# Kernel optimization log

Hardware: AMD Instinct MI355X
Metric: run time of the kernel (lower is better)

## Reference

```python
import jax, jax.numpy as jnp
import numpy as np

N_NODES = 100000
E = 1000000
IN_DIM = 64
HID = 64


def setup_inputs() -> dict:
    key = jax.random.key(0)
    ks = jax.random.split(key, 8)
    edge_emb = jax.random.normal(ks[0], (E, IN_DIM), dtype=jnp.float32)
    edge_indices = jax.random.randint(ks[1], (E, 2), 0, N_NODES, dtype=jnp.int64)
    s_in = 1.0 / np.sqrt(IN_DIM)
    s_h = 1.0 / np.sqrt(HID)
    Wf = jax.random.uniform(ks[2], (IN_DIM, HID), minval=-s_in, maxval=s_in, dtype=jnp.float32)
    bf = jax.random.uniform(ks[3], (HID,), minval=-s_in, maxval=s_in, dtype=jnp.float32)
    Wb = jax.random.uniform(ks[4], (IN_DIM, HID), minval=-s_in, maxval=s_in, dtype=jnp.float32)
    bb = jax.random.uniform(ks[5], (HID,), minval=-s_in, maxval=s_in, dtype=jnp.float32)
    Wg = jax.random.uniform(ks[6], (HID, 1), minval=-s_h, maxval=s_h, dtype=jnp.float32)
    bg = jax.random.uniform(ks[7], (1,), minval=-s_h, maxval=s_h, dtype=jnp.float32)
    return {"edge_emb": edge_emb, "Wf": Wf, "bf": bf, "Wb": Wb, "bb": bb,
            "Wg": Wg, "bg": bg, "edge_indices": edge_indices}


def reference(edge_emb, Wf, bf, Wb, bb, Wg, bg, edge_indices):
    u = edge_indices[:, 0]
    v = edge_indices[:, 1]
    # node_to_edges derived from incidence: sum of incident edge embeddings + degree
    node_sum = (jax.ops.segment_sum(edge_emb, u, num_segments=N_NODES)
                + jax.ops.segment_sum(edge_emb, v, num_segments=N_NODES))  # [N, d]
    ones = jnp.ones((edge_emb.shape[0],), edge_emb.dtype)
    deg = (jax.ops.segment_sum(ones, u, num_segments=N_NODES)
           + jax.ops.segment_sum(ones, v, num_segments=N_NODES))  # [N]

    def excl_mean(n):
        # mean over the node's incident edges excluding the current edge;
        # zeros when the current edge is the node's only incident edge.
        d = deg[n]                              # [E]
        s = node_sum[n] - edge_emb              # [E, d_in]
        denom = jnp.maximum(d - 1.0, 1.0)[:, None]
        return jnp.where((d > 1.0)[:, None], s / denom, jnp.zeros_like(s))

    agg_u = excl_mean(u)
    agg_v = excl_mean(v)
    agg_forward = agg_u @ Wf + bf               # [E, H]
    agg_backward = agg_v @ Wb + bb              # [E, H]
    gate = jax.nn.sigmoid((agg_forward + agg_backward) @ Wg + bg)  # [E, 1]
    return gate * agg_forward + (1.0 - gate) * agg_backward
```

## Files before the change

kernel.cpp:

```cpp
#include <hip/hip_runtime.h>
#include <hip/hip_bf16.h>
#include <math.h>

#define N_NODES 100000
#define DIM 64
#define BATCH 16
#define LDS_PITCH 72

typedef __attribute__((ext_vector_type(8))) short short8;
typedef __attribute__((ext_vector_type(4))) float floatx4;

__device__ __forceinline__ short f2bf(float x) {
    unsigned u = __float_as_uint(x);
    u += 0x7FFF + ((u >> 16) & 1);
    return (short)(u >> 16);
}
__device__ __forceinline__ float bf2f(unsigned short b) {
    return __uint_as_float(((unsigned)b) << 16);
}

__global__ __launch_bounds__(256) void scatter_kernel(
    const float* __restrict__ edge_emb, const int* __restrict__ idx,
    __hip_bfloat162* __restrict__ node_sum, float* __restrict__ deg, int n_edges)
{
    long long gid = (long long)blockIdx.x * blockDim.x + threadIdx.x;
    if (gid >= (long long)n_edges * 32) return;
    int e = (int)(gid >> 5);
    int p = (int)(gid & 31);
    float2 ev = ((const float2*)edge_emb)[gid];
    int2 uv = ((const int2*)idx)[e];
    union { unsigned u32; __hip_bfloat162 h; } cv;
    cv.u32 = (unsigned)(unsigned short)f2bf(ev.x)
           | ((unsigned)(unsigned short)f2bf(ev.y) << 16);
    unsafeAtomicAdd(&node_sum[(size_t)uv.x * 32 + p], cv.h);
    unsafeAtomicAdd(&node_sum[(size_t)uv.y * 32 + p], cv.h);
    if (p == 0) {
        unsafeAtomicAdd(&deg[uv.x], 1.f);
        unsafeAtomicAdd(&deg[uv.y], 1.f);
    }
}

__global__ __launch_bounds__(256) void fused_edge_kernel(
    const float* __restrict__ edge_emb,
    const int* __restrict__ idx,
    const unsigned short* __restrict__ node_sum,
    const float* __restrict__ deg,
    const float* __restrict__ Wf, const float* __restrict__ bf,
    const float* __restrict__ Wb, const float* __restrict__ bb,
    const float* __restrict__ Wg, const float* __restrict__ bg,
    float* __restrict__ out, int n_edges)
{
    __shared__ short lds[4][2][BATCH * LDS_PITCH];
    const int lane = threadIdx.x & 63;
    const int l15 = lane & 15;
    const int q = lane >> 4;
    const int wslot = threadIdx.x >> 6;
    const int wid = __builtin_amdgcn_readfirstlane(blockIdx.x * 4 + wslot);
    const int nwaves = gridDim.x * 4;

    short8 bWf[4][2], bWb[4][2];
#pragma unroll
    for (int nt = 0; nt < 4; ++nt)
#pragma unroll
        for (int kt = 0; kt < 2; ++kt) {
            short8 f, g;
#pragma unroll
            for (int j = 0; j < 8; ++j) {
                int k = kt * 32 + q * 8 + j;
                int n = nt * 16 + l15;
                f[j] = f2bf(Wf[k * 64 + n]);
                g[j] = f2bf(Wb[k * 64 + n]);
            }
            bWf[nt][kt] = f;
            bWb[nt][kt] = g;
        }
    float bfv[4], bbv[4], wgv[4];
#pragma unroll
    for (int nt = 0; nt < 4; ++nt) {
        bfv[nt] = bf[nt * 16 + l15];
        bbv[nt] = bb[nt * 16 + l15];
        wgv[nt] = Wg[nt * 16 + l15];
    }
    const float bgv = bg[0];

    short* ldsU = lds[wslot][0];
    short* ldsV = lds[wslot][1];

    const int nbatches = n_edges / BATCH;
    for (int b = wid; b < nbatches; b += nwaves) {
        const int e0 = b * BATCH;
#pragma unroll
        for (int i = 0; i < BATCH; ++i) {
            const int e = e0 + i;
            const int u = idx[2 * e];
            const int v = idx[2 * e + 1];
            const float du = deg[u];
            const float dv = deg[v];
            const float invu = (du > 1.f) ? 1.f / (du - 1.f) : 0.f;
            const float invv = (dv > 1.f) ? 1.f / (dv - 1.f) : 0.f;
            const float ev = edge_emb[(size_t)e * 64 + lane];
            const float nsu = bf2f(node_sum[(size_t)u * 64 + lane]);
            const float nsv = bf2f(node_sum[(size_t)v * 64 + lane]);
            ldsU[i * LDS_PITCH + lane] = f2bf((nsu - ev) * invu);
            ldsV[i * LDS_PITCH + lane] = f2bf((nsv - ev) * invv);
        }

        short8 aU[2], aV[2];
#pragma unroll
        for (int kt = 0; kt < 2; ++kt) {
            const int off = l15 * LDS_PITCH + kt * 32 + q * 8;
            aU[kt] = *(const short8*)&ldsU[off];
            aV[kt] = *(const short8*)&ldsV[off];
        }

        floatx4 cU[4], cV[4];
#pragma unroll
        for (int nt = 0; nt < 4; ++nt) {
            floatx4 z = {0.f, 0.f, 0.f, 0.f};
            z = __builtin_amdgcn_mfma_f32_16x16x32_bf16(aU[0], bWf[nt][0], z, 0, 0, 0);
            cU[nt] = __builtin_amdgcn_mfma_f32_16x16x32_bf16(aU[1], bWf[nt][1], z, 0, 0, 0);
            floatx4 z2 = {0.f, 0.f, 0.f, 0.f};
            z2 = __builtin_amdgcn_mfma_f32_16x16x32_bf16(aV[0], bWb[nt][0], z2, 0, 0, 0);
            cV[nt] = __builtin_amdgcn_mfma_f32_16x16x32_bf16(aV[1], bWb[nt][1], z2, 0, 0, 0);
        }

        float p[4] = {0.f, 0.f, 0.f, 0.f};
#pragma unroll
        for (int nt = 0; nt < 4; ++nt)
#pragma unroll
            for (int r = 0; r < 4; ++r) {
                float af = cU[nt][r] + bfv[nt];
                float ab = cV[nt][r] + bbv[nt];
                cU[nt][r] = af;
                cV[nt][r] = ab;
                p[r] = fmaf(af + ab, wgv[nt], p[r]);
            }
#pragma unroll
        for (int r = 0; r < 4; ++r) {
            float s = p[r];
            s += __shfl_xor(s, 1);
            s += __shfl_xor(s, 2);
            s += __shfl_xor(s, 4);
            s += __shfl_xor(s, 8);
            p[r] = 1.f / (1.f + __expf(-(s + bgv)));
        }
#pragma unroll
        for (int nt = 0; nt < 4; ++nt)
#pragma unroll
            for (int r = 0; r < 4; ++r) {
                const int e = e0 + q * 4 + r;
                out[(size_t)e * 64 + nt * 16 + l15] =
                    fmaf(p[r], cU[nt][r] - cV[nt][r], cV[nt][r]);
            }
    }
}

extern "C" void kernel_launch(void* const* d_in, const int* in_sizes, int n_in,
                              void* d_out, int out_size, void* d_ws, size_t ws_size,
                              hipStream_t stream) {
    const float* edge_emb = (const float*)d_in[0];
    const float* Wf = (const float*)d_in[1];
    const float* bf = (const float*)d_in[2];
    const float* Wb = (const float*)d_in[3];
    const float* bb = (const float*)d_in[4];
    const float* Wg = (const float*)d_in[5];
    const float* bg = (const float*)d_in[6];
    const int* idx = (const int*)d_in[7];
    float* out = (float*)d_out;

    const int n_edges = in_sizes[7] / 2;

    __hip_bfloat162* node_sum = (__hip_bfloat162*)d_ws;
    float* deg = (float*)((char*)d_ws + (size_t)N_NODES * DIM * 2);

    size_t zero_bytes = (size_t)N_NODES * DIM * 2 + (size_t)N_NODES * 4;
    hipMemsetAsync(d_ws, 0, zero_bytes, stream);

    long long sthreads = (long long)n_edges * 32;
    int blocks1 = (int)((sthreads + 255) / 256);
    scatter_kernel<<<blocks1, 256, 0, stream>>>(edge_emb, idx, node_sum, deg, n_edges);

    int blocks2 = 2048;
    fused_edge_kernel<<<blocks2, 256, 0, stream>>>(
        edge_emb, idx, (const unsigned short*)node_sum, deg,
        Wf, bf, Wb, bb, Wg, bg, out, n_edges);
}
```

Baseline: 891.3 us.

## Replace atomic bf16 scatter with bucketed per-node gather summation

```diff
diff --git a/kernel.cpp b/kernel.cpp
--- a/kernel.cpp
+++ b/kernel.cpp
@@ -40,6 +40,56 @@
     }
 }
 
+__global__ __launch_bounds__(256) void bucket_fill_kernel(
+    const int* __restrict__ idx, unsigned* __restrict__ cnt,
+    unsigned* __restrict__ bucket, int cap, int n_edges)
+{
+    int e = blockIdx.x * 256 + threadIdx.x;
+    if (e >= n_edges) return;
+    int2 uv = ((const int2*)idx)[e];
+    unsigned pu = atomicAdd(&cnt[uv.x], 1u);
+    if (pu < (unsigned)cap) bucket[(size_t)uv.x * cap + pu] = (unsigned)e;
+    unsigned pv = atomicAdd(&cnt[uv.y], 1u);
+    if (pv < (unsigned)cap) bucket[(size_t)uv.y * cap + pv] = (unsigned)e;
+}
+
+__global__ __launch_bounds__(256) void gather_sum_kernel(
+    const float* __restrict__ edge_emb, const unsigned* __restrict__ bucket,
+    const unsigned* __restrict__ cnt, unsigned short* __restrict__ node_sum,
+    float* __restrict__ degf, int cap)
+{
+    const int lane = threadIdx.x & 63;
+    const int wslot = threadIdx.x >> 6;
+    const int nwaves = gridDim.x * 4;
+    for (int n = blockIdx.x * 4 + wslot; n < N_NODES; n += nwaves) {
+        unsigned c = cnt[n];
+        if (c > (unsigned)cap) c = (unsigned)cap;
+        const unsigned* bptr = bucket + (size_t)n * cap;
+        float acc0 = 0.f, acc1 = 0.f, acc2 = 0.f, acc3 = 0.f;
+        for (unsigned base = 0; base < c; base += 64) {
+            int cc = (int)(c - base); if (cc > 64) cc = 64;
+            unsigned bv = (lane < cc) ? bptr[base + lane] : 0u;
+            int j = 0;
+            for (; j + 3 < cc; j += 4) {
+                unsigned e0 = (unsigned)__shfl((int)bv, j);
+                unsigned e1 = (unsigned)__shfl((int)bv, j + 1);
+                unsigned e2 = (unsigned)__shfl((int)bv, j + 2);
+                unsigned e3 = (unsigned)__shfl((int)bv, j + 3);
+                acc0 += edge_emb[(size_t)e0 * 64 + lane];
+                acc1 += edge_emb[(size_t)e1 * 64 + lane];
+                acc2 += edge_emb[(size_t)e2 * 64 + lane];
+                acc3 += edge_emb[(size_t)e3 * 64 + lane];
+            }
+            for (; j < cc; ++j) {
+                unsigned e0 = (unsigned)__shfl((int)bv, j);
+                acc0 += edge_emb[(size_t)e0 * 64 + lane];
+            }
+        }
+        node_sum[(size_t)n * 64 + lane] = (unsigned short)f2bf((acc0 + acc1) + (acc2 + acc3));
+        if (lane == 0) degf[n] = (float)c;
+    }
+}
+
 __global__ __launch_bounds__(256) void fused_edge_kernel(
     const float* __restrict__ edge_emb,
     const int* __restrict__ idx,
@@ -170,18 +220,36 @@
 
     const int n_edges = in_sizes[7] / 2;
 
-    __hip_bfloat162* node_sum = (__hip_bfloat162*)d_ws;
-    float* deg = (float*)((char*)d_ws + (size_t)N_NODES * DIM * 2);
-
-    size_t zero_bytes = (size_t)N_NODES * DIM * 2 + (size_t)N_NODES * 4;
-    hipMemsetAsync(d_ws, 0, zero_bytes, stream);
-
-    long long sthreads = (long long)n_edges * 32;
-    int blocks1 = (int)((sthreads + 255) / 256);
-    scatter_kernel<<<blocks1, 256, 0, stream>>>(edge_emb, idx, node_sum, deg, n_edges);
+    char* ws = (char*)d_ws;
+    const size_t ns_bytes  = (size_t)N_NODES * DIM * 2;
+    const size_t deg_bytes = (size_t)N_NODES * 4;
+    const size_t cnt_bytes = (size_t)N_NODES * 4;
+    unsigned short* node_sum = (unsigned short*)ws;
+    float* deg = (float*)(ws + ns_bytes);
+    unsigned* cnt = (unsigned*)(ws + ns_bytes + deg_bytes);
+    unsigned* bucket = (unsigned*)(ws + ns_bytes + deg_bytes + cnt_bytes);
+    const size_t fixed_bytes = ns_bytes + deg_bytes + cnt_bytes;
+
+    int cap = 0;
+    if (ws_size >= fixed_bytes + (size_t)N_NODES * 128 * 4)      cap = 128;
+    else if (ws_size >= fixed_bytes + (size_t)N_NODES * 64 * 4)  cap = 64;
+
+    if (cap) {
+        hipMemsetAsync(cnt, 0, cnt_bytes, stream);
+        int blocksF = (n_edges + 255) / 256;
+        bucket_fill_kernel<<<blocksF, 256, 0, stream>>>(idx, cnt, bucket, cap, n_edges);
+        gather_sum_kernel<<<2048, 256, 0, stream>>>(edge_emb, bucket, cnt,
+                                                    node_sum, deg, cap);
+    } else {
+        hipMemsetAsync(d_ws, 0, ns_bytes + deg_bytes, stream);
+        long long sthreads = (long long)n_edges * 32;
+        int blocks1 = (int)((sthreads + 255) / 256);
+        scatter_kernel<<<blocks1, 256, 0, stream>>>(edge_emb, idx,
+            (__hip_bfloat162*)node_sum, deg, n_edges);
+    }
 
     int blocks2 = 2048;
     fused_edge_kernel<<<blocks2, 256, 0, stream>>>(
-        edge_emb, idx, (const unsigned short*)node_sum, deg,
+        edge_emb, idx, node_sum, deg,
         Wf, bf, Wb, bb, Wg, bg, out, n_edges);
 }
```

Result: no change. 879.3 us (-1.4%).
